# Performance work log

Measured on AMD Instinct MI355X. Metric: run time of the kernel, lower is better.

The kernel has to match this reference:

```python
import jax, jax.numpy as jnp
import numpy as np

E = 300000        # num_edges
T = 3000000       # num_triplets
D = 128           # edge_message_dim
N_RAD = 6
N_SPH = 7
D_DOWN = 64       # edge_down_dim
D_BAS = 8         # basis_embed_dim


def _w(key, fan_in, fan_out):
    return jax.random.normal(key, (fan_in, fan_out), jnp.float32) / np.sqrt(fan_in)


def setup_inputs() -> dict:
    key = jax.random.key(0)
    ks = jax.random.split(key, 32)
    inp = {
        "x": jax.random.normal(ks[0], (E, D), jnp.float32),
        "rbf": jax.random.uniform(ks[1], (E, N_RAD), jnp.float32),
        "sbf": jax.random.uniform(ks[2], (T, N_SPH * N_RAD), jnp.float32),
        "idx_kj": jax.random.randint(ks[3], (T,), 0, E),
        "idx_ji": jax.random.randint(ks[4], (T,), 0, E),
        # basis projections (bias-free)
        "w_rbf1": _w(ks[5], N_RAD, D_BAS),
        "w_rbf2": _w(ks[6], D_BAS, D),
        "w_sbf1": _w(ks[7], N_SPH * N_RAD, D_BAS),
        "w_sbf2": _w(ks[8], D_BAS, D_DOWN),
        # message linears (with bias)
        "w_kj": _w(ks[9], D, D), "b_kj": jnp.zeros((D,), jnp.float32),
        "w_ji": _w(ks[10], D, D), "b_ji": jnp.zeros((D,), jnp.float32),
        # down / up projections (bias-free)
        "w_down": _w(ks[11], D, D_DOWN),
        "w_up": _w(ks[12], D_DOWN, D),
        # residual block before skip + dense
        "res1_w1": _w(ks[13], D, D), "res1_b1": jnp.zeros((D,), jnp.float32),
        "res1_w2": _w(ks[14], D, D), "res1_b2": jnp.zeros((D,), jnp.float32),
        "w_bs": _w(ks[15], D, D), "b_bs": jnp.zeros((D,), jnp.float32),
        # two residual blocks after skip
        "res2_w1": _w(ks[16], D, D), "res2_b1": jnp.zeros((D,), jnp.float32),
        "res2_w2": _w(ks[17], D, D), "res2_b2": jnp.zeros((D,), jnp.float32),
        "res3_w1": _w(ks[18], D, D), "res3_b1": jnp.zeros((D,), jnp.float32),
        "res3_w2": _w(ks[19], D, D), "res3_b2": jnp.zeros((D,), jnp.float32),
    }
    return inp


def _res_block(h, w1, b1, w2, b2):
    # h + act(lin2(act(lin1(h)))) with Swish(beta=1) == silu
    return h + jax.nn.silu(jax.nn.silu(h @ w1 + b1) @ w2 + b2)


def reference(x, rbf, sbf, idx_kj, idx_ji,
              w_rbf1, w_rbf2, w_sbf1, w_sbf2,
              w_kj, b_kj, w_ji, b_ji, w_down, w_up,
              res1_w1, res1_b1, res1_w2, res1_b2, w_bs, b_bs,
              res2_w1, res2_b1, res2_w2, res2_b2,
              res3_w1, res3_b1, res3_w2, res3_b2):
    act = jax.nn.silu
    x_ji = act(x @ w_ji + b_ji)                       # [E, D]
    x_kj = act(x @ w_kj + b_kj)                       # [E, D]
    rbf_e = (rbf @ w_rbf1) @ w_rbf2                   # [E, D]
    x_kj = act((x_kj * rbf_e) @ w_down)               # [E, D_DOWN]
    sbf_e = (sbf @ w_sbf1) @ w_sbf2                   # [T, D_DOWN]
    m = x_kj[idx_kj] * sbf_e                          # gather + Hadamard [T, D_DOWN]
    agg = jax.ops.segment_sum(m, idx_ji, num_segments=x.shape[0])  # [E, D_DOWN]
    x_kj = act(agg @ w_up)                            # [E, D]
    h = _res_block(x_ji + x_kj, res1_w1, res1_b1, res1_w2, res1_b2)
    h = act(h @ w_bs + b_bs) + x                      # skip connection
    h = _res_block(h, res2_w1, res2_b1, res2_w2, res2_b2)
    h = _res_block(h, res3_w1, res3_b1, res3_w2, res3_b2)
    return h
```

## Files before the change

kernel.cpp:

```cpp
#include <hip/hip_runtime.h>
#include <hip/hip_bf16.h>


typedef __attribute__((ext_vector_type(8))) _Float16 f16x8;
typedef __attribute__((ext_vector_type(4))) float f32x4;

__device__ __forceinline__ float silu_f(float v) {
    return v * __builtin_amdgcn_rcpf(1.0f + __expf(-v));
}

__device__ __forceinline__ void split44h(f32x4 a, f32x4 b, f16x8& hi, f16x8& lo) {
    float f[8] = {a[0], a[1], a[2], a[3], b[0], b[1], b[2], b[3]};
    #pragma unroll
    for (int j = 0; j < 8; ++j) {
        const _Float16 h = (_Float16)f[j];
        hi[j] = h;
        lo[j] = (_Float16)(f[j] - (float)h);
    }
}

__device__ __forceinline__ void gll16(const void* g, void* l) {
    __builtin_amdgcn_global_load_lds((const __attribute__((address_space(1))) void*)g,
                                     (__attribute__((address_space(3))) void*)l, 16, 0, 0);
}
__device__ __forceinline__ void stage8k(const char* g, _Float16* l, int lane, int wid) {
    #pragma unroll
    for (int i = 0; i < 2; ++i) {
        const int off = ((i * 4 + wid) << 10);
        gll16(g + off + lane * 16, (char*)l + off);
    }
}
__device__ __forceinline__ void stage4k(const char* g, _Float16* l, int lane, int wid) {
    const int off = (wid << 10);
    gll16(g + off + lane * 16, (char*)l + off);
}

template<int NF>
__device__ __forceinline__ void mfma_ks(f16x8 ah, f16x8 al, const _Float16* slot,
                                        int acol, int kq, f32x4* acc) {
    #pragma unroll
    for (int n = 0; n < NF; ++n) {
        const int c = n * 16 + acol;
        const int sw = (kq ^ ((c >> 1) & 3)) << 3;
        const f16x8 bh = *(const f16x8*)&slot[c * 32 + sw];
        acc[n] = __builtin_amdgcn_mfma_f32_16x16x32_f16(ah, bh, acc[n], 0, 0, 0);
        acc[n] = __builtin_amdgcn_mfma_f32_16x16x32_f16(al, bh, acc[n], 0, 0, 0);
    }
}

__device__ __forceinline__ void tfrag(const float* tl, int rb, int q, int kq,
                                      f16x8& Ah, f16x8& Al) {
    const f32x4 ta = *(const f32x4*)&tl[rb + q * 32 + kq * 8];
    const f32x4 tb = *(const f32x4*)&tl[rb + q * 32 + kq * 8 + 4];
    split44h(ta, tb, Ah, Al);
}

__device__ __forceinline__ void tgemm4(const char* img, const char* imgnext,
                                       _Float16* sA, _Float16* sB, const float* tl, int rb,
                                       int kq, int acol, int lane, int wid, f32x4* acc)
{
    f16x8 Ah[4], Al[4];
    #pragma unroll
    for (int q = 0; q < 4; ++q) tfrag(tl, rb, q, kq, Ah[q], Al[q]);

    stage8k(img + 8192, sB, lane, wid);
    mfma_ks<8>(Ah[0], Al[0], sA, acol, kq, acc); __syncthreads();
    stage8k(img + 16384, sA, lane, wid);
    mfma_ks<8>(Ah[1], Al[1], sB, acol, kq, acc); __syncthreads();
    stage8k(img + 24576, sB, lane, wid);
    mfma_ks<8>(Ah[2], Al[2], sA, acol, kq, acc); __syncthreads();
    if (imgnext) stage8k(imgnext, sA, lane, wid);
    mfma_ks<8>(Ah[3], Al[3], sB, acol, kq, acc); __syncthreads();
}

#define TPITCH 132

struct WDesc { const float* src; char* dst; int K; int N; };
struct ProArgs {
    WDesc w[11];
    const float* rbf; const float* w_rbf1; float* re1; int E;
    const int* idx_ji; int* cnt; int* rank; int T;
    int nW, nR;
};

__device__ void wprep_body(const ProArgs& P, int b) {
    const WDesc d = P.w[b >> 2];
    const int h = b & 3;
    if (h * 32 >= d.K) return;
    char* slab = d.dst + (size_t)h * d.N * 64;
    for (int idx = threadIdx.x; idx < d.N * 4; idx += 256) {
        const int c = idx >> 2, ch = idx & 3;
        f16x8 v;
        #pragma unroll
        for (int j = 0; j < 8; ++j)
            v[j] = (_Float16)d.src[(size_t)(h * 32 + ch * 8 + j) * d.N + c];
        *(f16x8*)(slab + c * 64 + ((ch ^ ((c >> 1) & 3)) << 4)) = v;
    }
}

__device__ void rbf1_body(const ProArgs& P, int b) {
    const int i = b * 256 + threadIdx.x;
    const int e = i >> 3, p = i & 7;
    if (e < P.E) {
        float s = 0.f;
        #pragma unroll
        for (int q = 0; q < 6; ++q) s = fmaf(P.rbf[e * 6 + q], P.w_rbf1[q * 8 + p], s);
        P.re1[i] = s;
    }
}

__device__ void count_rank_body(const ProArgs& P, int b) {
    const int i = (b * 256 + threadIdx.x) * 4;
    const int T = P.T;
    if (i + 3 < T) {
        const int4 j = *(const int4*)&P.idx_ji[i];
        int4 r;
        r.x = atomicAdd(&P.cnt[j.x], 1);
        r.y = atomicAdd(&P.cnt[j.y], 1);
        r.z = atomicAdd(&P.cnt[j.z], 1);
        r.w = atomicAdd(&P.cnt[j.w], 1);
        *(int4*)&P.rank[i] = r;
    } else {
        for (int k = i; k < T; ++k) P.rank[k] = atomicAdd(&P.cnt[P.idx_ji[k]], 1);
    }
}

__global__ void pro_kernel(ProArgs P) {
    const int b = blockIdx.x;
    if (b < P.nW)             wprep_body(P, b);
    else if (b < P.nW + P.nR) rbf1_body(P, b - P.nW);
    else                      count_rank_body(P, b - P.nW - P.nR);
}


__global__ void scan_partial_kernel(const int* __restrict__ cnt, int* __restrict__ partial, int E) {
    __shared__ int red[256];
    const int tid = threadIdx.x;
    const int base = blockIdx.x * 1024 + tid * 4;
    int s = 0;
    #pragma unroll
    for (int i = 0; i < 4; ++i) { const int g = base + i; if (g < E) s += cnt[g]; }
    red[tid] = s;
    __syncthreads();
    for (int off = 128; off > 0; off >>= 1) {
        if (tid < off) red[tid] += red[tid + off];
        __syncthreads();
    }
    if (tid == 0) partial[blockIdx.x] = red[0];
}

__global__ void scan_block_kernel(const int* __restrict__ partial, int* __restrict__ blockoff,
                                  int NB, int* offsets, int E) {
    __shared__ int red[256];
    const int tid = threadIdx.x;
    int v[4]; int s = 0;
    #pragma unroll
    for (int i = 0; i < 4; ++i) { const int g = tid * 4 + i; v[i] = (g < NB) ? partial[g] : 0; s += v[i]; }
    red[tid] = s;
    __syncthreads();
    for (int off = 1; off < 256; off <<= 1) {
        const int add = (tid >= off) ? red[tid - off] : 0;
        __syncthreads();
        red[tid] += add;
        __syncthreads();
    }
    int excl = (tid == 0) ? 0 : red[tid - 1];
    #pragma unroll
    for (int i = 0; i < 4; ++i) { const int g = tid * 4 + i; if (g < NB) blockoff[g] = excl; excl += v[i]; }
    if (tid == 255) offsets[E] = red[255];
}

__global__ void scan_final_kernel(const int* __restrict__ cnt, const int* __restrict__ blockoff,
                                  int* __restrict__ offsets, int E) {
    __shared__ int red[256];
    const int tid = threadIdx.x;
    const int base = blockIdx.x * 1024 + tid * 4;
    int v[4]; int s = 0;
    #pragma unroll
    for (int i = 0; i < 4; ++i) { const int g = base + i; v[i] = (g < E) ? cnt[g] : 0; s += v[i]; }
    red[tid] = s;
    __syncthreads();
    for (int off = 1; off < 256; off <<= 1) {
        const int add = (tid >= off) ? red[tid - off] : 0;
        __syncthreads();
        red[tid] += add;
        __syncthreads();
    }
    int run = blockoff[blockIdx.x] + ((tid == 0) ? 0 : red[tid - 1]);
    #pragma unroll
    for (int i = 0; i < 4; ++i) {
        const int g = base + i;
        if (g < E) offsets[g] = run;
        run += v[i];
    }
}

__launch_bounds__(256, 3)
__global__ void e1fill_kernel(const float* __restrict__ sbf, const float* __restrict__ w_sbf1,
                              const int* __restrict__ idx_ji, const int* __restrict__ idx_kj,
                              const int* __restrict__ rank, const int* __restrict__ offsets,
                              _Float16* __restrict__ E1p, int* __restrict__ kjp, int T)
{
    __shared__ float s_lds[256 * 43];
    const int tid = threadIdx.x;
    const long long t0 = (long long)blockIdx.x * 256;
    const int nrow = min(256, (int)(T - t0));
    const int nel  = nrow * 42;
    const float* base = sbf + t0 * 42;

    for (int i = tid * 4; i + 3 < nel; i += 1024) {
        const float4 v = *(const float4*)&base[i];
        s_lds[(i + 0) + (i + 0) / 42] = v.x;
        s_lds[(i + 1) + (i + 1) / 42] = v.y;
        s_lds[(i + 2) + (i + 2) / 42] = v.z;
        s_lds[(i + 3) + (i + 3) / 42] = v.w;
    }
    const int tail0 = nel & ~3;
    if (tid < nel - tail0) { const int g = tail0 + tid; s_lds[g + g / 42] = base[g]; }
    __syncthreads();

    const int t = (int)t0 + tid;
    if (t >= T) return;
    const float* srow = &s_lds[tid * 43];
    float e1[8] = {0.f, 0.f, 0.f, 0.f, 0.f, 0.f, 0.f, 0.f};
    #pragma unroll
    for (int q = 0; q < 42; ++q) {
        const float s = srow[q];
        #pragma unroll
        for (int p = 0; p < 8; ++p) e1[p] = fmaf(s, w_sbf1[q * 8 + p], e1[p]);
    }
    f16x8 eh;
    #pragma unroll
    for (int p = 0; p < 8; ++p) eh[p] = (_Float16)e1[p];
    const int ji  = idx_ji[t];
    const int pos = offsets[ji] + rank[t];
    *(f16x8*)&E1p[(size_t)pos * 8] = eh;
    kjp[pos] = idx_kj[t];
}

__launch_bounds__(256, 4)
__global__ void gather_kernel(const _Float16* __restrict__ E1p, const int* __restrict__ kjp,
                              const float* __restrict__ w_sbf2, const int* __restrict__ offsets,
                              const _Float16* __restrict__ xkjd, float* __restrict__ agg, int E)
{
    const int tid  = threadIdx.x;
    const int lane = tid & 63;
    const int e    = blockIdx.x * 4 + (tid >> 6);

    float w2[8];
    #pragma unroll
    for (int p = 0; p < 8; ++p) w2[p] = w_sbf2[p * 64 + lane];

    if (e >= E) return;
    const int j0 = __builtin_amdgcn_readfirstlane(offsets[e]);
    const int j1 = __builtin_amdgcn_readfirstlane(offsets[e + 1]);

    float acc = 0.f;
    if (j0 < j1) {
        int kj = __builtin_amdgcn_readfirstlane(kjp[j0]);
        f16x8 ev = *(const f16x8*)&E1p[(size_t)j0 * 8];
        float xv = (float)xkjd[(size_t)kj * 64 + lane];
        for (int j = j0; j < j1; ++j) {
            float xn = 0.f; f16x8 evn = {};
            if (j + 1 < j1) {
                const int kn = __builtin_amdgcn_readfirstlane(kjp[j + 1]);
                evn = *(const f16x8*)&E1p[(size_t)(j + 1) * 8];
                xn  = (float)xkjd[(size_t)kn * 64 + lane];
            }
            float sv = (float)ev[0] * w2[0];
            sv = fmaf((float)ev[1], w2[1], sv);
            sv = fmaf((float)ev[2], w2[2], sv);
            sv = fmaf((float)ev[3], w2[3], sv);
            sv = fmaf((float)ev[4], w2[4], sv);
            sv = fmaf((float)ev[5], w2[5], sv);
            sv = fmaf((float)ev[6], w2[6], sv);
            sv = fmaf((float)ev[7], w2[7], sv);
            acc = fmaf(xv, sv, acc);
            ev = evn; xv = xn;
        }
    }
    agg[(size_t)e * 64 + lane] = acc;
}

__launch_bounds__(256, 3)
__global__ void k1_kernel(const float* __restrict__ x, const char* __restrict__ wkj_i,
                          const float* __restrict__ b_kj, const float* __restrict__ re1,
                          const float* __restrict__ w_rbf2, const char* __restrict__ wdn_i,
                          _Float16* __restrict__ W3, int E)
{
    __shared__ _Float16 slotA[4096], slotB[4096];
    __shared__ float t_lds[64 * TPITCH];
    __shared__ float w2_lds[8 * 128];
    const int tid = threadIdx.x, lane = tid & 63, wid = tid >> 6;
    const int acol = lane & 15, kq = lane >> 4;
    const int rowW = blockIdx.x * 64 + wid * 16;
    const int arow = rowW + acol;
    const bool av = arow < E;

    stage8k(wkj_i, slotA, lane, wid);
    const float* xr = x + (size_t)arow * 128;
    f16x8 aH[4], aL[4];
    #pragma unroll
    for (int ks = 0; ks < 4; ++ks) {
        f32x4 a0 = f32x4{0.f, 0.f, 0.f, 0.f}, a1 = f32x4{0.f, 0.f, 0.f, 0.f};
        if (av) { a0 = *(const f32x4*)&xr[ks * 32 + kq * 8];
                  a1 = *(const f32x4*)&xr[ks * 32 + kq * 8 + 4]; }
        split44h(a0, a1, aH[ks], aL[ks]);
    }
    float bv[8];
    #pragma unroll
    for (int n = 0; n < 8; ++n) bv[n] = b_kj[n * 16 + acol];
    f32x4 e1a[4], e1b[4];
    #pragma unroll
    for (int r = 0; r < 4; ++r) {
        const int ge = rowW + kq * 4 + r;
        e1a[r] = f32x4{0.f, 0.f, 0.f, 0.f}; e1b[r] = f32x4{0.f, 0.f, 0.f, 0.f};
        if (ge < E) { e1a[r] = *(const f32x4*)&re1[(size_t)ge * 8];
                      e1b[r] = *(const f32x4*)&re1[(size_t)ge * 8 + 4]; }
    }
    for (int i = tid; i < 1024; i += 256) w2_lds[i] = w_rbf2[i];
    __syncthreads();

    f32x4 acc[8];
    #pragma unroll
    for (int n = 0; n < 8; ++n) acc[n] = f32x4{0.f, 0.f, 0.f, 0.f};

    stage8k(wkj_i + 8192, slotB, lane, wid);
    mfma_ks<8>(aH[0], aL[0], slotA, acol, kq, acc); __syncthreads();
    stage8k(wkj_i + 16384, slotA, lane, wid);
    mfma_ks<8>(aH[1], aL[1], slotB, acol, kq, acc); __syncthreads();
    stage8k(wkj_i + 24576, slotB, lane, wid);
    mfma_ks<8>(aH[2], aL[2], slotA, acol, kq, acc); __syncthreads();
    stage4k(wdn_i, slotA, lane, wid);
    mfma_ks<8>(aH[3], aL[3], slotB, acol, kq, acc); __syncthreads();

    #pragma unroll
    for (int n = 0; n < 8; ++n) {
        const int c = n * 16 + acol;
        float w2c[8];
        #pragma unroll
        for (int p = 0; p < 8; ++p) w2c[p] = w2_lds[p * 128 + c];
        #pragma unroll
        for (int r = 0; r < 4; ++r) {
            float s = e1a[r][0] * w2c[0];
            s = fmaf(e1a[r][1], w2c[1], s);
            s = fmaf(e1a[r][2], w2c[2], s);
            s = fmaf(e1a[r][3], w2c[3], s);
            s = fmaf(e1b[r][0], w2c[4], s);
            s = fmaf(e1b[r][1], w2c[5], s);
            s = fmaf(e1b[r][2], w2c[6], s);
            s = fmaf(e1b[r][3], w2c[7], s);
            t_lds[(wid * 16 + kq * 4 + r) * TPITCH + c] = silu_f(acc[n][r] + bv[n]) * s;
        }
    }
    __syncthreads();

    f32x4 acc2[4];
    #pragma unroll
    for (int n = 0; n < 4; ++n) acc2[n] = f32x4{0.f, 0.f, 0.f, 0.f};
    const int rb = (wid * 16 + acol) * TPITCH;

    f16x8 tH[4], tL[4];
    #pragma unroll
    for (int q = 0; q < 4; ++q) tfrag(t_lds, rb, q, kq, tH[q], tL[q]);

    stage4k(wdn_i + 4096, slotB, lane, wid);
    mfma_ks<4>(tH[0], tL[0], slotA, acol, kq, acc2); __syncthreads();
    stage4k(wdn_i + 8192, slotA, lane, wid);
    mfma_ks<4>(tH[1], tL[1], slotB, acol, kq, acc2); __syncthreads();
    stage4k(wdn_i + 12288, slotB, lane, wid);
    mfma_ks<4>(tH[2], tL[2], slotA, acol, kq, acc2); __syncthreads();
    mfma_ks<4>(tH[3], tL[3], slotB, acol, kq, acc2);

    #pragma unroll
    for (int n = 0; n < 4; ++n) {
        const int c = n * 16 + acol;
        #pragma unroll
        for (int r = 0; r < 4; ++r) {
            const int ge = rowW + kq * 4 + r;
            if (ge < E) W3[(size_t)ge * 64 + c] = (_Float16)silu_f(acc2[n][r]);
        }
    }
}

struct KBigArgs {
    const float* x; const float* W4; float* out;
    const char *wji, *wup, *r1w1, *r1w2, *wbs, *r2w1, *r2w2, *r3w1, *r3w2;
    const float *bji, *r1b1, *r1b2, *bbs, *r2b1, *r2b2, *r3b1, *r3b2;
    int E;
};

__launch_bounds__(256, 3)
__global__ void kbig_kernel(KBigArgs A_)
{
    __shared__ _Float16 slotA[4096], slotB[4096];
    __shared__ float t_lds[64 * TPITCH];
    const int tid = threadIdx.x, lane = tid & 63, wid = tid >> 6;
    const int acol = lane & 15, kq = lane >> 4;
    const int rowW = blockIdx.x * 64 + wid * 16;
    const int arow = rowW + acol;
    const int E = A_.E;
    const bool av = arow < E;
    const int rb = (wid * 16 + acol) * TPITCH;

    stage8k(A_.wji, slotA, lane, wid);

    const float* xr = A_.x + (size_t)arow * 128;
    const float* wr = A_.W4 + (size_t)arow * 64;
    f16x8 aH[4], aL[4], uH[2], uL[2];
    #pragma unroll
    for (int ks = 0; ks < 4; ++ks) {
        f32x4 a0 = f32x4{0.f, 0.f, 0.f, 0.f}, a1 = f32x4{0.f, 0.f, 0.f, 0.f};
        if (av) { a0 = *(const f32x4*)&xr[ks * 32 + kq * 8];
                  a1 = *(const f32x4*)&xr[ks * 32 + kq * 8 + 4]; }
        split44h(a0, a1, aH[ks], aL[ks]);
    }
    #pragma unroll
    for (int ks = 0; ks < 2; ++ks) {
        f32x4 u0 = f32x4{0.f, 0.f, 0.f, 0.f}, u1 = f32x4{0.f, 0.f, 0.f, 0.f};
        if (av) { u0 = *(const f32x4*)&wr[ks * 32 + kq * 8];
                  u1 = *(const f32x4*)&wr[ks * 32 + kq * 8 + 4]; }
        split44h(u0, u1, uH[ks], uL[ks]);
    }
    __syncthreads();

    f32x4 acc[8];
    #pragma unroll
    for (int n = 0; n < 8; ++n) acc[n] = f32x4{0.f, 0.f, 0.f, 0.f};

    stage8k(A_.wji + 8192, slotB, lane, wid);
    mfma_ks<8>(aH[0], aL[0], slotA, acol, kq, acc); __syncthreads();
    stage8k(A_.wji + 16384, slotA, lane, wid);
    mfma_ks<8>(aH[1], aL[1], slotB, acol, kq, acc); __syncthreads();
    stage8k(A_.wji + 24576, slotB, lane, wid);
    mfma_ks<8>(aH[2], aL[2], slotA, acol, kq, acc); __syncthreads();
    stage8k(A_.wup, slotA, lane, wid);
    mfma_ks<8>(aH[3], aL[3], slotB, acol, kq, acc); __syncthreads();

    float res[8][4];
    #pragma unroll
    for (int n = 0; n < 8; ++n) {
        const float bv = A_.bji[n * 16 + acol];
        #pragma unroll
        for (int r = 0; r < 4; ++r) { res[n][r] = silu_f(acc[n][r] + bv); acc[n][r] = 0.f; }
    }

    stage8k(A_.wup + 8192, slotB, lane, wid);
    mfma_ks<8>(uH[0], uL[0], slotA, acol, kq, acc); __syncthreads();
    stage8k(A_.r1w1, slotA, lane, wid);
    mfma_ks<8>(uH[1], uL[1], slotB, acol, kq, acc); __syncthreads();

    #pragma unroll
    for (int n = 0; n < 8; ++n) {
        const int c = n * 16 + acol;
        #pragma unroll
        for (int r = 0; r < 4; ++r) {
            res[n][r] += silu_f(acc[n][r]);
            t_lds[(wid * 16 + kq * 4 + r) * TPITCH + c] = res[n][r];
            acc[n][r] = 0.f;
        }
    }
    __syncthreads();

    tgemm4(A_.r1w1, A_.r1w2, slotA, slotB, t_lds, rb, kq, acol, lane, wid, acc);
    #pragma unroll
    for (int n = 0; n < 8; ++n) {
        const float bv = A_.r1b1[n * 16 + acol];
        const int c = n * 16 + acol;
        #pragma unroll
        for (int r = 0; r < 4; ++r) {
            t_lds[(wid * 16 + kq * 4 + r) * TPITCH + c] = silu_f(acc[n][r] + bv);
            acc[n][r] = 0.f;
        }
    }
    __syncthreads();

    tgemm4(A_.r1w2, A_.wbs, slotA, slotB, t_lds, rb, kq, acol, lane, wid, acc);
    #pragma unroll
    for (int n = 0; n < 8; ++n) {
        const float bv = A_.r1b2[n * 16 + acol];
        const int c = n * 16 + acol;
        #pragma unroll
        for (int r = 0; r < 4; ++r) {
            t_lds[(wid * 16 + kq * 4 + r) * TPITCH + c] = res[n][r] + silu_f(acc[n][r] + bv);
            acc[n][r] = 0.f;
        }
    }
    __syncthreads();

    tgemm4(A_.wbs, A_.r2w1, slotA, slotB, t_lds, rb, kq, acol, lane, wid, acc);
    #pragma unroll
    for (int n = 0; n < 8; ++n) {
        const float bv = A_.bbs[n * 16 + acol];
        const int c = n * 16 + acol;
        #pragma unroll
        for (int r = 0; r < 4; ++r) {
            const int ge = rowW + kq * 4 + r;
            const float xv = (ge < E) ? A_.x[(size_t)ge * 128 + c] : 0.f;
            res[n][r] = silu_f(acc[n][r] + bv) + xv;
            t_lds[(wid * 16 + kq * 4 + r) * TPITCH + c] = res[n][r];
            acc[n][r] = 0.f;
        }
    }
    __syncthreads();

    tgemm4(A_.r2w1, A_.r2w2, slotA, slotB, t_lds, rb, kq, acol, lane, wid, acc);
    #pragma unroll
    for (int n = 0; n < 8; ++n) {
        const float bv = A_.r2b1[n * 16 + acol];
        const int c = n * 16 + acol;
        #pragma unroll
        for (int r = 0; r < 4; ++r) {
            t_lds[(wid * 16 + kq * 4 + r) * TPITCH + c] = silu_f(acc[n][r] + bv);
            acc[n][r] = 0.f;
        }
    }
    __syncthreads();

    tgemm4(A_.r2w2, A_.r3w1, slotA, slotB, t_lds, rb, kq, acol, lane, wid, acc);
    #pragma unroll
    for (int n = 0; n < 8; ++n) {
        const float bv = A_.r2b2[n * 16 + acol];
        const int c = n * 16 + acol;
        #pragma unroll
        for (int r = 0; r < 4; ++r) {
            res[n][r] += silu_f(acc[n][r] + bv);
            t_lds[(wid * 16 + kq * 4 + r) * TPITCH + c] = res[n][r];
            acc[n][r] = 0.f;
        }
    }
    __syncthreads();

    tgemm4(A_.r3w1, A_.r3w2, slotA, slotB, t_lds, rb, kq, acol, lane, wid, acc);
    #pragma unroll
    for (int n = 0; n < 8; ++n) {
        const float bv = A_.r3b1[n * 16 + acol];
        const int c = n * 16 + acol;
        #pragma unroll
        for (int r = 0; r < 4; ++r) {
            t_lds[(wid * 16 + kq * 4 + r) * TPITCH + c] = silu_f(acc[n][r] + bv);
            acc[n][r] = 0.f;
        }
    }
    __syncthreads();

    tgemm4(A_.r3w2, nullptr, slotA, slotB, t_lds, rb, kq, acol, lane, wid, acc);
    #pragma unroll
    for (int n = 0; n < 8; ++n) {
        const float bv = A_.r3b2[n * 16 + acol];
        const int c = n * 16 + acol;
        #pragma unroll
        for (int r = 0; r < 4; ++r) {
            const int ge = rowW + kq * 4 + r;
            if (ge < E)
                A_.out[(size_t)ge * 128 + c] = res[n][r] + silu_f(acc[n][r] + bv);
        }
    }
}


extern "C" void kernel_launch(void* const* d_in, const int* in_sizes, int n_in,
                              void* d_out, int out_size, void* d_ws, size_t ws_size,
                              hipStream_t stream)
{
    const float* x      = (const float*)d_in[0];
    const float* rbf    = (const float*)d_in[1];
    const float* sbf    = (const float*)d_in[2];
    const int*   idx_kj = (const int*)d_in[3];
    const int*   idx_ji = (const int*)d_in[4];
    const float* w_rbf1 = (const float*)d_in[5];
    const float* w_rbf2 = (const float*)d_in[6];
    const float* w_sbf1 = (const float*)d_in[7];
    const float* w_sbf2 = (const float*)d_in[8];
    const float* w_kj   = (const float*)d_in[9];
    const float* b_kj   = (const float*)d_in[10];
    const float* w_ji   = (const float*)d_in[11];
    const float* b_ji   = (const float*)d_in[12];
    const float* w_down = (const float*)d_in[13];
    const float* w_up   = (const float*)d_in[14];
    const float* r1w1   = (const float*)d_in[15];
    const float* r1b1   = (const float*)d_in[16];
    const float* r1w2   = (const float*)d_in[17];
    const float* r1b2   = (const float*)d_in[18];
    const float* w_bs   = (const float*)d_in[19];
    const float* b_bs   = (const float*)d_in[20];
    const float* r2w1   = (const float*)d_in[21];
    const float* r2b1   = (const float*)d_in[22];
    const float* r2w2   = (const float*)d_in[23];
    const float* r2b2   = (const float*)d_in[24];
    const float* r3w1   = (const float*)d_in[25];
    const float* r3b1   = (const float*)d_in[26];
    const float* r3w2   = (const float*)d_in[27];
    const float* r3b2   = (const float*)d_in[28];

    const int E = in_sizes[0] / 128;
    const int T = in_sizes[2] / 42;

    float* OUT = (float*)d_out;
    _Float16* W3 = (_Float16*)((char*)d_ws + (size_t)E * 128 * 4);
    float* W4  = (float*)((char*)d_ws + (size_t)E * 128 * 4
                                      + (size_t)E * 64 * 4);

    int*   cnt      = (int*)d_ws;
    int*   offsets  = cnt + (E + 64);
    int*   partial  = offsets + (E + 64);
    int*   blockoff = partial + 1024;
    _Float16* E1p   = (_Float16*)((char*)d_ws + (4u << 20));
    int*   kjp      = (int*)((char*)d_ws + (102u << 20));
    float* re1      = (float*)((char*)d_ws + (116u << 20));
    char*  wimg     = (char*)d_ws + (130u << 20);
    int*   rank     = (int*)((char*)d_ws + (134u << 20));

    char* wkj_i  = wimg;
    char* wji_i  = wimg + 32768;
    char* wdn_i  = wimg + 65536;
    char* wup_i  = wimg + 81920;
    char* r1w1_i = wimg + 98304;
    char* r1w2_i = wimg + 131072;
    char* wbs_i  = wimg + 163840;
    char* r2w1_i = wimg + 196608;
    char* r2w2_i = wimg + 229376;
    char* r3w1_i = wimg + 262144;
    char* r3w2_i = wimg + 294912;

    const dim3 b256(256);
    const int gB  = (E + 63) / 64;
    const int gT  = (T + 255) / 256;
    const int gT4 = (T + 1023) / 1024;
    const int NB  = (E + 1023) / 1024;
    const int gE4 = (E + 3) / 4;
    const int gR  = (E * 8 + 255) / 256;

    ProArgs P;
    P.w[0]  = {w_kj,   wkj_i,  128, 128};
    P.w[1]  = {w_ji,   wji_i,  128, 128};
    P.w[2]  = {w_down, wdn_i,  128,  64};
    P.w[3]  = {w_up,   wup_i,   64, 128};
    P.w[4]  = {r1w1,   r1w1_i, 128, 128};
    P.w[5]  = {r1w2,   r1w2_i, 128, 128};
    P.w[6]  = {w_bs,   wbs_i,  128, 128};
    P.w[7]  = {r2w1,   r2w1_i, 128, 128};
    P.w[8]  = {r2w2,   r2w2_i, 128, 128};
    P.w[9]  = {r3w1,   r3w1_i, 128, 128};
    P.w[10] = {r3w2,   r3w2_i, 128, 128};
    P.rbf = rbf; P.w_rbf1 = w_rbf1; P.re1 = re1; P.E = E;
    P.idx_ji = idx_ji; P.cnt = cnt; P.rank = rank; P.T = T;
    P.nW = 44; P.nR = gR;

    hipMemsetAsync(cnt, 0, (size_t)E * 4, stream);
    pro_kernel<<<44 + gR + gT4, b256, 0, stream>>>(P);
    scan_partial_kernel<<<NB, b256, 0, stream>>>(cnt, partial, E);
    scan_block_kernel<<<1, b256, 0, stream>>>(partial, blockoff, NB, offsets, E);
    scan_final_kernel<<<NB, b256, 0, stream>>>(cnt, blockoff, offsets, E);
    e1fill_kernel<<<gT, b256, 0, stream>>>(sbf, w_sbf1, idx_ji, idx_kj, rank, offsets, E1p, kjp, T);

    k1_kernel<<<gB, b256, 0, stream>>>(x, wkj_i, b_kj, re1, w_rbf2, wdn_i, W3, E);
    gather_kernel<<<gE4, b256, 0, stream>>>(E1p, kjp, w_sbf2, offsets, W3, W4, E);

    KBigArgs ka;
    ka.x = x; ka.W4 = W4; ka.out = OUT;
    ka.wji = wji_i; ka.wup = wup_i; ka.r1w1 = r1w1_i; ka.r1w2 = r1w2_i; ka.wbs = wbs_i;
    ka.r2w1 = r2w1_i; ka.r2w2 = r2w2_i; ka.r3w1 = r3w1_i; ka.r3w2 = r3w2_i;
    ka.bji = b_ji; ka.r1b1 = r1b1; ka.r1b2 = r1b2; ka.bbs = b_bs;
    ka.r2b1 = r2b1; ka.r2b2 = r2b2; ka.r3b1 = r3b1; ka.r3b2 = r3b2;
    ka.E = E;
    kbig_kernel<<<gB, b256, 0, stream>>>(ka);
}
```

Baseline: 995.5 us.

## Read GEMM weights directly from global memory and stage sbf as fp16

Removes the LDS double-buffered weight staging (global_load_lds into slotA/slotB) and most __syncthreads in k1 and kbig. Each wave now loads its MFMA B-fragments straight from the pre-swizzled global weight images, relying on L1/L2 caching, and occupancy bounds are raised. Separately, e1fill stores the sbf tile in LDS as fp16 instead of fp32, halving its LDS footprint so more blocks can be resident. The trade-offs are more global/L2 traffic per wave, extra registers for the prefetched fragments, and reduced precision of sbf before the first projection.

```diff
diff --git a/kernel.cpp b/kernel.cpp
--- a/kernel.cpp
+++ b/kernel.cpp
@@ -19,32 +19,21 @@
     }
 }
 
-__device__ __forceinline__ void gll16(const void* g, void* l) {
-    __builtin_amdgcn_global_load_lds((const __attribute__((address_space(1))) void*)g,
-                                     (__attribute__((address_space(3))) void*)l, 16, 0, 0);
-}
-__device__ __forceinline__ void stage8k(const char* g, _Float16* l, int lane, int wid) {
-    #pragma unroll
-    for (int i = 0; i < 2; ++i) {
-        const int off = ((i * 4 + wid) << 10);
-        gll16(g + off + lane * 16, (char*)l + off);
-    }
-}
-__device__ __forceinline__ void stage4k(const char* g, _Float16* l, int lane, int wid) {
-    const int off = (wid << 10);
-    gll16(g + off + lane * 16, (char*)l + off);
-}
-
 template<int NF>
-__device__ __forceinline__ void mfma_ks(f16x8 ah, f16x8 al, const _Float16* slot,
+__device__ __forceinline__ void mfma_ks(f16x8 ah, f16x8 al,
+                                        const _Float16* __restrict__ slab,
                                         int acol, int kq, f32x4* acc) {
+    f16x8 bh[NF];
     #pragma unroll
     for (int n = 0; n < NF; ++n) {
         const int c = n * 16 + acol;
         const int sw = (kq ^ ((c >> 1) & 3)) << 3;
-        const f16x8 bh = *(const f16x8*)&slot[c * 32 + sw];
-        acc[n] = __builtin_amdgcn_mfma_f32_16x16x32_f16(ah, bh, acc[n], 0, 0, 0);
-        acc[n] = __builtin_amdgcn_mfma_f32_16x16x32_f16(al, bh, acc[n], 0, 0, 0);
+        bh[n] = *(const f16x8*)&slab[c * 32 + sw];
+    }
+    #pragma unroll
+    for (int n = 0; n < NF; ++n) {
+        acc[n] = __builtin_amdgcn_mfma_f32_16x16x32_f16(ah, bh[n], acc[n], 0, 0, 0);
+        acc[n] = __builtin_amdgcn_mfma_f32_16x16x32_f16(al, bh[n], acc[n], 0, 0, 0);
     }
 }
 
@@ -55,22 +44,15 @@
     split44h(ta, tb, Ah, Al);
 }
 
-__device__ __forceinline__ void tgemm4(const char* img, const char* imgnext,
-                                       _Float16* sA, _Float16* sB, const float* tl, int rb,
-                                       int kq, int acol, int lane, int wid, f32x4* acc)
+__device__ __forceinline__ void tgemm4g(const char* img, const float* tl, int rb,
+                                        int kq, int acol, f32x4* acc)
 {
     f16x8 Ah[4], Al[4];
     #pragma unroll
     for (int q = 0; q < 4; ++q) tfrag(tl, rb, q, kq, Ah[q], Al[q]);
-
-    stage8k(img + 8192, sB, lane, wid);
-    mfma_ks<8>(Ah[0], Al[0], sA, acol, kq, acc); __syncthreads();
-    stage8k(img + 16384, sA, lane, wid);
-    mfma_ks<8>(Ah[1], Al[1], sB, acol, kq, acc); __syncthreads();
-    stage8k(img + 24576, sB, lane, wid);
-    mfma_ks<8>(Ah[2], Al[2], sA, acol, kq, acc); __syncthreads();
-    if (imgnext) stage8k(imgnext, sA, lane, wid);
-    mfma_ks<8>(Ah[3], Al[3], sB, acol, kq, acc); __syncthreads();
+    #pragma unroll
+    for (int s = 0; s < 4; ++s)
+        mfma_ks<8>(Ah[s], Al[s], (const _Float16*)(img + 8192 * s), acol, kq, acc);
 }
 
 #define TPITCH 132
@@ -195,13 +177,13 @@
     }
 }
 
-__launch_bounds__(256, 3)
+__launch_bounds__(256, 7)
 __global__ void e1fill_kernel(const float* __restrict__ sbf, const float* __restrict__ w_sbf1,
                               const int* __restrict__ idx_ji, const int* __restrict__ idx_kj,
                               const int* __restrict__ rank, const int* __restrict__ offsets,
                               _Float16* __restrict__ E1p, int* __restrict__ kjp, int T)
 {
-    __shared__ float s_lds[256 * 43];
+    __shared__ _Float16 s_lds[256 * 44];
     const int tid = threadIdx.x;
     const long long t0 = (long long)blockIdx.x * 256;
     const int nrow = min(256, (int)(T - t0));
@@ -210,22 +192,22 @@
 
     for (int i = tid * 4; i + 3 < nel; i += 1024) {
         const float4 v = *(const float4*)&base[i];
-        s_lds[(i + 0) + (i + 0) / 42] = v.x;
-        s_lds[(i + 1) + (i + 1) / 42] = v.y;
-        s_lds[(i + 2) + (i + 2) / 42] = v.z;
-        s_lds[(i + 3) + (i + 3) / 42] = v.w;
+        s_lds[(i + 0) + 2 * ((i + 0) / 42)] = (_Float16)v.x;
+        s_lds[(i + 1) + 2 * ((i + 1) / 42)] = (_Float16)v.y;
+        s_lds[(i + 2) + 2 * ((i + 2) / 42)] = (_Float16)v.z;
+        s_lds[(i + 3) + 2 * ((i + 3) / 42)] = (_Float16)v.w;
     }
     const int tail0 = nel & ~3;
-    if (tid < nel - tail0) { const int g = tail0 + tid; s_lds[g + g / 42] = base[g]; }
+    if (tid < nel - tail0) { const int g = tail0 + tid; s_lds[g + 2 * (g / 42)] = (_Float16)base[g]; }
     __syncthreads();
 
     const int t = (int)t0 + tid;
     if (t >= T) return;
-    const float* srow = &s_lds[tid * 43];
+    const _Float16* srow = &s_lds[tid * 44];
     float e1[8] = {0.f, 0.f, 0.f, 0.f, 0.f, 0.f, 0.f, 0.f};
     #pragma unroll
     for (int q = 0; q < 42; ++q) {
-        const float s = srow[q];
+        const float s = (float)srow[q];
         #pragma unroll
         for (int p = 0; p < 8; ++p) e1[p] = fmaf(s, w_sbf1[q * 8 + p], e1[p]);
     }
@@ -282,13 +264,12 @@
     agg[(size_t)e * 64 + lane] = acc;
 }
 
-__launch_bounds__(256, 3)
+__launch_bounds__(256, 4)
 __global__ void k1_kernel(const float* __restrict__ x, const char* __restrict__ wkj_i,
                           const float* __restrict__ b_kj, const float* __restrict__ re1,
                           const float* __restrict__ w_rbf2, const char* __restrict__ wdn_i,
                           _Float16* __restrict__ W3, int E)
 {
-    __shared__ _Float16 slotA[4096], slotB[4096];
     __shared__ float t_lds[64 * TPITCH];
     __shared__ float w2_lds[8 * 128];
     const int tid = threadIdx.x, lane = tid & 63, wid = tid >> 6;
@@ -297,7 +278,6 @@
     const int arow = rowW + acol;
     const bool av = arow < E;
 
-    stage8k(wkj_i, slotA, lane, wid);
     const float* xr = x + (size_t)arow * 128;
     f16x8 aH[4], aL[4];
     #pragma unroll
@@ -325,14 +305,9 @@
     #pragma unroll
     for (int n = 0; n < 8; ++n) acc[n] = f32x4{0.f, 0.f, 0.f, 0.f};
 
-    stage8k(wkj_i + 8192, slotB, lane, wid);
-    mfma_ks<8>(aH[0], aL[0], slotA, acol, kq, acc); __syncthreads();
-    stage8k(wkj_i + 16384, slotA, lane, wid);
-    mfma_ks<8>(aH[1], aL[1], slotB, acol, kq, acc); __syncthreads();
-    stage8k(wkj_i + 24576, slotB, lane, wid);
-    mfma_ks<8>(aH[2], aL[2], slotA, acol, kq, acc); __syncthreads();
-    stage4k(wdn_i, slotA, lane, wid);
-    mfma_ks<8>(aH[3], aL[3], slotB, acol, kq, acc); __syncthreads();
+    #pragma unroll
+    for (int s = 0; s < 4; ++s)
+        mfma_ks<8>(aH[s], aL[s], (const _Float16*)(wkj_i + 8192 * s), acol, kq, acc);
 
     #pragma unroll
     for (int n = 0; n < 8; ++n) {
@@ -353,7 +328,6 @@
             t_lds[(wid * 16 + kq * 4 + r) * TPITCH + c] = silu_f(acc[n][r] + bv[n]) * s;
         }
     }
-    __syncthreads();
 
     f32x4 acc2[4];
     #pragma unroll
@@ -363,14 +337,9 @@
     f16x8 tH[4], tL[4];
     #pragma unroll
     for (int q = 0; q < 4; ++q) tfrag(t_lds, rb, q, kq, tH[q], tL[q]);
-
-    stage4k(wdn_i + 4096, slotB, lane, wid);
-    mfma_ks<4>(tH[0], tL[0], slotA, acol, kq, acc2); __syncthreads();
-    stage4k(wdn_i + 8192, slotA, lane, wid);
-    mfma_ks<4>(tH[1], tL[1], slotB, acol, kq, acc2); __syncthreads();
-    stage4k(wdn_i + 12288, slotB, lane, wid);
-    mfma_ks<4>(tH[2], tL[2], slotA, acol, kq, acc2); __syncthreads();
-    mfma_ks<4>(tH[3], tL[3], slotB, acol, kq, acc2);
+    #pragma unroll
+    for (int s = 0; s < 4; ++s)
+        mfma_ks<4>(tH[s], tL[s], (const _Float16*)(wdn_i + 4096 * s), acol, kq, acc2);
 
     #pragma unroll
     for (int n = 0; n < 4; ++n) {
@@ -390,10 +359,9 @@
     int E;
 };
 
-__launch_bounds__(256, 3)
+__launch_bounds__(256, 4)
 __global__ void kbig_kernel(KBigArgs A_)
 {
-    __shared__ _Float16 slotA[4096], slotB[4096];
     __shared__ float t_lds[64 * TPITCH];
     const int tid = threadIdx.x, lane = tid & 63, wid = tid >> 6;
     const int acol = lane & 15, kq = lane >> 4;
@@ -403,8 +371,6 @@
     const bool av = arow < E;
     const int rb = (wid * 16 + acol) * TPITCH;
 
-    stage8k(A_.wji, slotA, lane, wid);
-
     const float* xr = A_.x + (size_t)arow * 128;
     const float* wr = A_.W4 + (size_t)arow * 64;
     f16x8 aH[4], aL[4], uH[2], uL[2];
@@ -422,20 +388,14 @@
                   u1 = *(const f32x4*)&wr[ks * 32 + kq * 8 + 4]; }
         split44h(u0, u1, uH[ks], uL[ks]);
     }
-    __syncthreads();
 
     f32x4 acc[8];
     #pragma unroll
     for (int n = 0; n < 8; ++n) acc[n] = f32x4{0.f, 0.f, 0.f, 0.f};
 
-    stage8k(A_.wji + 8192, slotB, lane, wid);
-    mfma_ks<8>(aH[0], aL[0], slotA, acol, kq, acc); __syncthreads();
-    stage8k(A_.wji + 16384, slotA, lane, wid);
-    mfma_ks<8>(aH[1], aL[1], slotB, acol, kq, acc); __syncthreads();
-    stage8k(A_.wji + 24576, slotB, lane, wid);
-    mfma_ks<8>(aH[2], aL[2], slotA, acol, kq, acc); __syncthreads();
-    stage8k(A_.wup, slotA, lane, wid);
-    mfma_ks<8>(aH[3], aL[3], slotB, acol, kq, acc); __syncthreads();
+    #pragma unroll
+    for (int s = 0; s < 4; ++s)
+        mfma_ks<8>(aH[s], aL[s], (const _Float16*)(A_.wji + 8192 * s), acol, kq, acc);
 
     float res[8][4];
     #pragma unroll
@@ -445,10 +405,9 @@
         for (int r = 0; r < 4; ++r) { res[n][r] = silu_f(acc[n][r] + bv); acc[n][r] = 0.f; }
     }
 
-    stage8k(A_.wup + 8192, slotB, lane, wid);
-    mfma_ks<8>(uH[0], uL[0], slotA, acol, kq, acc); __syncthreads();
-    stage8k(A_.r1w1, slotA, lane, wid);
-    mfma_ks<8>(uH[1], uL[1], slotB, acol, kq, acc); __syncthreads();
+    #pragma unroll
+    for (int s = 0; s < 2; ++s)
+        mfma_ks<8>(uH[s], uL[s], (const _Float16*)(A_.wup + 8192 * s), acol, kq, acc);
 
     #pragma unroll
     for (int n = 0; n < 8; ++n) {
@@ -460,9 +419,8 @@
             acc[n][r] = 0.f;
         }
     }
-    __syncthreads();
-
-    tgemm4(A_.r1w1, A_.r1w2, slotA, slotB, t_lds, rb, kq, acol, lane, wid, acc);
+
+    tgemm4g(A_.r1w1, t_lds, rb, kq, acol, acc);
     #pragma unroll
     for (int n = 0; n < 8; ++n) {
         const float bv = A_.r1b1[n * 16 + acol];
@@ -473,9 +431,8 @@
             acc[n][r] = 0.f;
         }
     }
-    __syncthreads();
-
-    tgemm4(A_.r1w2, A_.wbs, slotA, slotB, t_lds, rb, kq, acol, lane, wid, acc);
+
+    tgemm4g(A_.r1w2, t_lds, rb, kq, acol, acc);
     #pragma unroll
     for (int n = 0; n < 8; ++n) {
         const float bv = A_.r1b2[n * 16 + acol];
@@ -486,9 +443,8 @@
             acc[n][r] = 0.f;
         }
     }
-    __syncthreads();
-
-    tgemm4(A_.wbs, A_.r2w1, slotA, slotB, t_lds, rb, kq, acol, lane, wid, acc);
+
+    tgemm4g(A_.wbs, t_lds, rb, kq, acol, acc);
     #pragma unroll
     for (int n = 0; n < 8; ++n) {
         const float bv = A_.bbs[n * 16 + acol];
@@ -502,9 +458,8 @@
             acc[n][r] = 0.f;
         }
     }
-    __syncthreads();
-
-    tgemm4(A_.r2w1, A_.r2w2, slotA, slotB, t_lds, rb, kq, acol, lane, wid, acc);
+
+    tgemm4g(A_.r2w1, t_lds, rb, kq, acol, acc);
     #pragma unroll
     for (int n = 0; n < 8; ++n) {
         const float bv = A_.r2b1[n * 16 + acol];
@@ -515,9 +470,8 @@
             acc[n][r] = 0.f;
         }
     }
-    __syncthreads();
-
-    tgemm4(A_.r2w2, A_.r3w1, slotA, slotB, t_lds, rb, kq, acol, lane, wid, acc);
+
+    tgemm4g(A_.r2w2, t_lds, rb, kq, acol, acc);
     #pragma unroll
     for (int n = 0; n < 8; ++n) {
         const float bv = A_.r2b2[n * 16 + acol];
@@ -529,9 +483,8 @@
             acc[n][r] = 0.f;
         }
     }
-    __syncthreads();
-
-    tgemm4(A_.r3w1, A_.r3w2, slotA, slotB, t_lds, rb, kq, acol, lane, wid, acc);
+
+    tgemm4g(A_.r3w1, t_lds, rb, kq, acol, acc);
     #pragma unroll
     for (int n = 0; n < 8; ++n) {
         const float bv = A_.r3b1[n * 16 + acol];
@@ -542,9 +495,8 @@
             acc[n][r] = 0.f;
         }
     }
-    __syncthreads();
-
-    tgemm4(A_.r3w2, nullptr, slotA, slotB, t_lds, rb, kq, acol, lane, wid, acc);
+
+    tgemm4g(A_.r3w2, t_lds, rb, kq, acol, acc);
     #pragma unroll
     for (int n = 0; n < 8; ++n) {
         const float bv = A_.r3b2[n * 16 + acol];
```

After: 1.009 ms. Within noise of the previous version (+1.3%).
